# Optimization experiments

Hardware: AMD Instinct MI355X
Metric: run time of the kernel (lower is better)

The kernel has to match this reference:

```python
import jax, jax.numpy as jnp
import numpy as np

V = 1.0      # SinReLU scale (gin-configurable)
EPS = 1e-5   # LayerNorm eps

def sinrelu(x):
    return jnp.where(x >= 0, (x + jnp.sin(x)) * V, jnp.zeros_like(x))

def _cell(x, h, p):
    # ELTMcell: fused gated recurrent step. torch Linear weights are [out, in].
    gates = x @ p['xi'].T + h @ p['hi'].T + p['bhi']          # [B, 2H]
    i_g, h_g = jnp.split(gates, 2, axis=-1)
    ch = jax.nn.sigmoid(i_g) * jnp.tanh(h_g)                  # candidate hidden
    xn = jnp.tanh(x @ p['ox'].T)                              # only_x path
    hn = jnp.tanh(h @ p['oh'].T)                              # only_h path
    o = jax.nn.sigmoid(xn @ p['io'].T + hn @ p['ho'].T + ch @ p['cho'].T + p['bcho'])
    a = o @ p['a'].T
    b = o @ p['b'].T
    return a * xn + b * hn + (1.0 - a - b) * ch

def _forward(x, p0, p1, ln_g, ln_b):
    B = x.shape[1]
    H = p0['hi'].shape[1]
    def step(carry, xt):
        h0, h1 = carry
        h0 = _cell(xt, h0, p0)
        h1 = _cell(h0, h1, p1)
        return (h0, h1), h1
    init = (jnp.zeros((B, H), x.dtype), jnp.zeros((B, H), x.dtype))
    _, out = jax.lax.scan(step, init, x)      # [S, B, H]
    out = sinrelu(out)                        # dropout = identity (eval mode)
    mu = jnp.mean(out, axis=-1, keepdims=True)
    var = jnp.var(out, axis=-1, keepdims=True)
    return (out - mu) * jax.lax.rsqrt(var + EPS) * ln_g + ln_b

def setup_inputs() -> dict:
    S, B, D, H = 512, 128, 128, 512   # seq_len, batch, layer_size, hidden = multiple*layer_size
    keys = iter(jax.random.split(jax.random.key(0), 40))
    def w(o, i):
        return jax.random.normal(next(keys), (o, i), jnp.float32) * 0.05
    def bvec(o):
        return jax.random.normal(next(keys), (o,), jnp.float32) * 0.05
    inp = {'x': jax.random.normal(next(keys), (S, B, D), jnp.float32)}
    for l, din in ((0, D), (1, H)):
        inp[f'w{l}_xi'] = w(2 * H, din)
        inp[f'w{l}_hi'] = w(2 * H, H)
        inp[f'b{l}_hi'] = bvec(2 * H)
        inp[f'w{l}_ox'] = w(H, din)
        inp[f'w{l}_oh'] = w(H, H)
        inp[f'w{l}_io'] = w(H, H)
        inp[f'w{l}_ho'] = w(H, H)
        inp[f'w{l}_cho'] = w(H, H)
        inp[f'b{l}_cho'] = bvec(H)
        inp[f'w{l}_a'] = w(H, H)
        inp[f'w{l}_b'] = w(H, H)
    inp['ln_g'] = jnp.ones((H,), jnp.float32)
    inp['ln_b'] = jnp.zeros((H,), jnp.float32)
    return inp

def reference(x, w0_xi, w0_hi, b0_hi, w0_ox, w0_oh, w0_io, w0_ho, w0_cho, b0_cho, w0_a, w0_b,
              w1_xi, w1_hi, b1_hi, w1_ox, w1_oh, w1_io, w1_ho, w1_cho, b1_cho, w1_a, w1_b,
              ln_g, ln_b):
    p0 = dict(xi=w0_xi, hi=w0_hi, bhi=b0_hi, ox=w0_ox, oh=w0_oh, io=w0_io, ho=w0_ho,
              cho=w0_cho, bcho=b0_cho, a=w0_a, b=w0_b)
    p1 = dict(xi=w1_xi, hi=w1_hi, bhi=b1_hi, ox=w1_ox, oh=w1_oh, io=w1_io, ho=w1_ho,
              cho=w1_cho, bcho=b1_cho, a=w1_a, b=w1_b)
    return _forward(x, p0, p1, ln_g, ln_b)
```

## Files before the change

kernel.cpp:

```cpp
#include <hip/hip_runtime.h>
#include <hip/hip_bf16.h>

#define S_ 512
#define B_ 128
#define D_ 128
#define H_ 512
#define NB_ 256

#define PK_SA 159744
#define PK_B  5111808
#define PK_BS 98304
#define PK_C  8257536
#define PK_CS 65536
#define PK_TOT 10354688
#define APLANE 65536
#define ASZ    131072

#define SC1 4.8828125e-4f
#define SC2 2.384185791015625e-7f

typedef short bf16x8 __attribute__((ext_vector_type(8)));
typedef _Float16 f16x8 __attribute__((ext_vector_type(8)));
typedef int i32x4 __attribute__((ext_vector_type(4)));
typedef float f32x4 __attribute__((ext_vector_type(4)));

__device__ __forceinline__ float sigf(float x) { return 1.0f / (1.0f + expf(-x)); }

__device__ __forceinline__ i32x4 ldg(const short* p) {
  i32x4 o;
  asm volatile("global_load_dwordx4 %0, %1, off" : "=v"(o) : "v"(p));
  return o;
}
#define VMDRAIN()                                    \
  do {                                               \
    asm volatile("s_waitcnt vmcnt(0)" ::: "memory"); \
    __builtin_amdgcn_sched_barrier(0);               \
  } while (0)

__device__ __forceinline__ void st2(short* buf, int idx, float v) {
  _Float16 h0 = (_Float16)v;
  float r1 = (v - (float)h0) * 2048.0f;
  _Float16 h1 = (_Float16)r1;
  buf[idx] = __builtin_bit_cast(short, h0);
  buf[idx + APLANE] = __builtin_bit_cast(short, h1);
}
__device__ __forceinline__ float ld2p(const short* buf, int idx) {
  float a = (float)__builtin_bit_cast(_Float16, buf[idx]);
  float b = (float)__builtin_bit_cast(_Float16, buf[idx + APLANE]);
  return a + b * SC1;
}

#define MFMAH(a, b, c) __builtin_amdgcn_mfma_f32_16x16x32_f16(a, b, c, 0, 0, 0)
#define BC16(x) __builtin_bit_cast(f16x8, x)

__device__ __forceinline__ void mac4(f32x4& c0, f32x4& c1, f32x4& c2, const f16x8& a0,
                                     const f16x8& a1, const f16x8& w0, const f16x8& w1) {
  c0 = MFMAH(a0, w0, c0);
  c1 = MFMAH(a0, w1, c1);
  c1 = MFMAH(a1, w0, c1);
  c2 = MFMAH(a1, w1, c2);
}
__device__ __forceinline__ f32x4 fin3(const f32x4& c0, const f32x4& c1,
                                      const f32x4& c2) {
  f32x4 o;
#pragma unroll
  for (int e = 0; e < 4; ++e) o[e] = c0[e] + SC1 * c1[e] + SC2 * c2[e];
  return o;
}

__device__ __forceinline__ void unitP(f32x4& c0, f32x4& c1, f32x4& c2,
                                      const short* aBase, const short* slab, int nks,
                                      int lo) {
  for (int q = 0; q < nks; q += 4) {
    i32x4 A0[4], A1[4], W0[4], W1[4];
#pragma unroll
    for (int u = 0; u < 4; ++u) {
      const short* wp = slab + (size_t)(q + u) * 1024 + lo;
      W0[u] = ldg(wp);
      W1[u] = ldg(wp + 512);
      const short* ap = aBase + (q + u) * 32;
      A0[u] = ldg(ap);
      A1[u] = ldg(ap + APLANE);
    }
    VMDRAIN();
#pragma unroll
    for (int u = 0; u < 4; ++u)
      mac4(c0, c1, c2, BC16(A0[u]), BC16(A1[u]), BC16(W0[u]), BC16(W1[u]));
  }
}

__device__ __forceinline__ void unitPx(f32x4& c0, f32x4& c1, f32x4& c2,
                                       const float* xRow, const short* slab, int lo) {
  i32x4 W0[4], W1[4];
  f16x8 A0[4], A1[4];
#pragma unroll
  for (int u = 0; u < 4; ++u) {
    const short* wp = slab + (size_t)u * 1024 + lo;
    W0[u] = ldg(wp);
    W1[u] = ldg(wp + 512);
#pragma unroll
    for (int e = 0; e < 8; ++e) {
      float v = xRow[u * 32 + e];
      _Float16 h0 = (_Float16)v;
      A0[u][e] = h0;
      A1[u][e] = (_Float16)((v - (float)h0) * 2048.0f);
    }
  }
  VMDRAIN();
#pragma unroll
  for (int u = 0; u < 4; ++u) mac4(c0, c1, c2, A0[u], A1[u], BC16(W0[u]), BC16(W1[u]));
}

__device__ __forceinline__ unsigned int afa(unsigned int* p) {
  return __hip_atomic_fetch_add(p, 1u, __ATOMIC_RELAXED, __HIP_MEMORY_SCOPE_AGENT);
}
__device__ __forceinline__ unsigned int ald(const unsigned int* p) {
  return __hip_atomic_load(p, __ATOMIC_RELAXED, __HIP_MEMORY_SCOPE_AGENT);
}

__device__ __forceinline__ void gbarX(unsigned int* ctl, int xcd, unsigned int bt,
                                      unsigned int m) {
  asm volatile("s_waitcnt vmcnt(0) lgkmcnt(0)" ::: "memory");
  __syncthreads();
  if (threadIdx.x == 0) {
    unsigned int o = afa(&ctl[32 + 32 * xcd]);
    if (o == m * bt - 1)
      afa(&ctl[48 + 32 * xcd]);
    else
      while (ald(&ctl[48 + 32 * xcd]) < bt) __builtin_amdgcn_s_sleep(2);
  }
  __syncthreads();
  asm volatile("buffer_inv sc0" ::: "memory");
  __builtin_amdgcn_sched_barrier(0);
}

struct PP {
  const float* x;
  const short* pw;
  short* h0s;
  short* h1s;
  short* xn0;
  short* hn0;
  short* ch0;
  short* xn1;
  short* hn1;
  short* ch1;
  short* o0;
  short* o1;
  const float* bhi0;
  const float* bcho0;
  const float* bhi1;
  const float* bcho1;
  float* out;
  unsigned int* ctl;
};

__global__ __launch_bounds__(512, 1) void eltm_p(PP p) {
  extern __shared__ char smem[];
  float* ldsF = (float*)smem;
  unsigned int* shI = (unsigned int*)(smem + 16384);
  const int tid = threadIdx.x;
  const int lane = tid & 63;
  const int w = tid >> 6;
  const int r = lane & 15;
  const int g = lane >> 4;
  const int lo = r * 32 + g * 8;
  const f32x4 z = {0.f, 0.f, 0.f, 0.f};

  unsigned int xcd;
  asm volatile("s_getreg_b32 %0, hwreg(HW_REG_XCC_ID)" : "=s"(xcd));
  xcd &= 7;
  const int sgx = ((int)xcd) << 2;

  if (tid == 0) {
    shI[0] = afa(&p.ctl[xcd]);
    unsigned int o = afa(&p.ctl[8]);
    if (o == NB_ - 1)
      __hip_atomic_store(&p.ctl[9], 1u, __ATOMIC_RELAXED, __HIP_MEMORY_SCOPE_AGENT);
    while (ald(&p.ctl[9]) == 0) __builtin_amdgcn_s_sleep(2);
    shI[1] = ald(&p.ctl[xcd]);
  }
  __syncthreads();
  const int slot = shI[0];
  const unsigned int m = shI[1];
  asm volatile("buffer_inv sc0" ::: "memory");

  const int row0 = (int)xcd * 16;
  const int aoff = (row0 + r) * H_ + g * 8;
  static const int preW[8] = {0, 20480, 40960, 45056, 61440, 94208, 126976, 143360};

  unsigned int bt = 0;
  for (int i = 0; i <= S_; ++i) {
    const int do0 = i < S_;
    const int do1 = i >= 1;
    const float* xr = p.x + ((size_t)i * B_ + row0 + r) * D_ + g * 8;

    for (int t = slot; t < 32; t += (int)m) {
      const int s = (t + sgx) & 31;
      const short* slabA = p.pw + (size_t)s * PK_SA;
      const int n = s * 16 + r;
      f32x4 c0 = z, c1 = z, c2 = z;
      f32x4 fin = z;
      switch (w) {
        case 0:
        case 1:
          if (do0) {
            const short* sl = slabA + preW[w];
            unitPx(c0, c1, c2, xr, sl, lo);
            unitP(c0, c1, c2, p.h0s + aoff, sl + 4096, 16, lo);
            fin = fin3(c0, c1, c2);
          }
          break;
        case 2:
          if (do0) {
            unitPx(c0, c1, c2, xr, slabA + preW[2], lo);
            fin = fin3(c0, c1, c2);
#pragma unroll
            for (int e = 0; e < 4; ++e)
              st2(p.xn0, (row0 + g * 4 + e) * H_ + n, tanhf(fin[e]));
          }
          break;
        case 3:
          if (do0) {
            unitP(c0, c1, c2, p.h0s + aoff, slabA + preW[3], 16, lo);
            fin = fin3(c0, c1, c2);
#pragma unroll
            for (int e = 0; e < 4; ++e)
              st2(p.hn0, (row0 + g * 4 + e) * H_ + n, tanhf(fin[e]));
          }
          break;
        case 4:
        case 5:
          if (do1) {
            const short* sl = slabA + preW[w];
            unitP(c0, c1, c2, p.h0s + aoff, sl, 16, lo);
            unitP(c0, c1, c2, p.h1s + aoff, sl + 16384, 16, lo);
            fin = fin3(c0, c1, c2);
          }
          break;
        case 6:
          if (do1) {
            unitP(c0, c1, c2, p.h0s + aoff, slabA + preW[6], 16, lo);
            fin = fin3(c0, c1, c2);
#pragma unroll
            for (int e = 0; e < 4; ++e)
              st2(p.xn1, (row0 + g * 4 + e) * H_ + n, tanhf(fin[e]));
          }
          break;
        default:
          if (do1) {
            unitP(c0, c1, c2, p.h1s + aoff, slabA + preW[7], 16, lo);
            fin = fin3(c0, c1, c2);
#pragma unroll
            for (int e = 0; e < 4; ++e)
              st2(p.hn1, (row0 + g * 4 + e) * H_ + n, tanhf(fin[e]));
          }
          break;
      }
      if ((w == 1 && do0) || (w == 5 && do1)) {
#pragma unroll
        for (int e = 0; e < 4; ++e)
          ldsF[(w == 5 ? 256 : 0) + (g * 4 + e) * 16 + r] = fin[e];
      }
      __syncthreads();
      if (w == 0 && do0) {
        const float bi = p.bhi0[n], bh = p.bhi0[512 + n];
#pragma unroll
        for (int e = 0; e < 4; ++e) {
          float hgv = ldsF[(g * 4 + e) * 16 + r];
          st2(p.ch0, (row0 + g * 4 + e) * H_ + n, sigf(fin[e] + bi) * tanhf(hgv + bh));
        }
      }
      if (w == 4 && do1) {
        const float bi = p.bhi1[n], bh = p.bhi1[512 + n];
#pragma unroll
        for (int e = 0; e < 4; ++e) {
          float hgv = ldsF[256 + (g * 4 + e) * 16 + r];
          st2(p.ch1, (row0 + g * 4 + e) * H_ + n, sigf(fin[e] + bi) * tanhf(hgv + bh));
        }
      }
      __syncthreads();
    }
    ++bt;
    gbarX(p.ctl, xcd, bt, m);

    for (int t = slot; t < 32; t += (int)m) {
      const int s = (t + sgx) & 31;
      const int L = w >> 2;
      const int tt = w & 3;
      const int ok = L ? do1 : do0;
      const int n = s * 16 + r;
      if (ok) {
        f32x4 c0 = z, c1 = z, c2 = z;
        const short* slab = p.pw + PK_B + (size_t)s * PK_BS + (size_t)L * 49152;
        const short* xn = L ? p.xn1 : p.xn0;
        const short* hn = L ? p.hn1 : p.hn0;
        const short* ch = L ? p.ch1 : p.ch0;
        if (tt == 0)
          unitP(c0, c1, c2, xn + aoff, slab, 16, lo);
        else if (tt == 1)
          unitP(c0, c1, c2, hn + aoff, slab + 16384, 16, lo);
        else if (tt == 2)
          unitP(c0, c1, c2, ch + aoff, slab + 32768, 8, lo);
        else
          unitP(c0, c1, c2, ch + aoff + 256, slab + 40960, 8, lo);
        f32x4 fin = fin3(c0, c1, c2);
#pragma unroll
        for (int e = 0; e < 4; ++e) ldsF[w * 256 + (g * 4 + e) * 16 + r] = fin[e];
      }
      __syncthreads();
      if ((w == 0 && do0) || (w == 4 && do1)) {
        const float bc = (w == 4 ? p.bcho1 : p.bcho0)[n];
        short* o = w == 4 ? p.o1 : p.o0;
#pragma unroll
        for (int e = 0; e < 4; ++e) {
          const int q = (g * 4 + e) * 16 + r;
          float sum = ldsF[w * 256 + q] + ldsF[(w + 1) * 256 + q] +
                      ldsF[(w + 2) * 256 + q] + ldsF[(w + 3) * 256 + q];
          st2(o, (row0 + g * 4 + e) * H_ + n, sigf(sum + bc));
        }
      }
      __syncthreads();
    }
    ++bt;
    gbarX(p.ctl, xcd, bt, m);

    for (int t = slot; t < 32; t += (int)m) {
      const int s = (t + sgx) & 31;
      const int L = s & 1;
      const int ok = L ? do1 : do0;
      const int u = w >> 1;
      const int h = w & 1;
      if (ok) {
        f32x4 c0 = z, c1 = z, c2 = z;
        const short* slab =
            p.pw + PK_C + (size_t)s * PK_CS + (size_t)u * 16384 + (size_t)h * 8192;
        const short* o = L ? p.o1 : p.o0;
        unitP(c0, c1, c2, o + aoff + h * 256, slab, 8, lo);
        f32x4 fin = fin3(c0, c1, c2);
#pragma unroll
        for (int e = 0; e < 4; ++e) ldsF[w * 256 + (g * 4 + e) * 16 + r] = fin[e];
      }
      __syncthreads();
      if ((w == 0 || w == 4) && ok) {
        const int j = (w == 0) ? (s >> 1) : (16 + (s >> 1));
        const int ub = (w == 0) ? 0 : 4;
        const short* xn = L ? p.xn1 : p.xn0;
        const short* hn = L ? p.hn1 : p.hn0;
        const short* ch = L ? p.ch1 : p.ch0;
        short* hs = L ? p.h1s : p.h0s;
#pragma unroll
        for (int e = 0; e < 4; ++e) {
          const int q = (g * 4 + e) * 16 + r;
          const float av = ldsF[(ub + 0) * 256 + q] + ldsF[(ub + 1) * 256 + q];
          const float bv = ldsF[(ub + 2) * 256 + q] + ldsF[(ub + 3) * 256 + q];
          const int idx = (row0 + g * 4 + e) * H_ + j * 16 + r;
          const float hval = av * ld2p(xn, idx) + bv * ld2p(hn, idx) +
                             (1.f - av - bv) * ld2p(ch, idx);
          st2(hs, idx, hval);
          if (L) p.out[(size_t)(i - 1) * B_ * H_ + idx] = hval;
        }
      }
      __syncthreads();
    }
    ++bt;
    gbarX(p.ctl, xcd, bt, m);
  }
}

struct WP18 {
  const float* m[18];
};
__global__ void repack(WP18 wp, short* pw) {
  const long long t8 = (long long)blockIdx.x * 256 + threadIdx.x;
  const long long id = t8 * 8;
  if (id >= (long long)PK_TOT) return;
  int mat, row, kb, p;
  if (id < (long long)PK_B) {
    int s = (int)(id / PK_SA), rem = (int)(id % PK_SA);
    const int pre[9] = {0, 20480, 40960, 45056, 61440, 94208, 126976, 143360, 159744};
    int w = 0;
    while (rem >= pre[w + 1]) ++w;
    int off = rem - pre[w];
    int c = off >> 10, r2 = off & 1023;
    p = r2 >> 9;
    int q2 = r2 & 511, rr = q2 >> 5, gg = (q2 & 31) >> 3;
    int kin = c * 32 + gg * 8;
    switch (w) {
      case 0:
      case 1:
        row = (w == 1 ? 512 : 0) + s * 16 + rr;
        if (kin < 128) { mat = 0; kb = kin; } else { mat = 1; kb = kin - 128; }
        break;
      case 2: mat = 2; row = s * 16 + rr; kb = kin; break;
      case 3: mat = 3; row = s * 16 + rr; kb = kin; break;
      case 4:
      case 5:
        row = (w == 5 ? 512 : 0) + s * 16 + rr;
        if (kin < 512) { mat = 9; kb = kin; } else { mat = 10; kb = kin - 512; }
        break;
      case 6: mat = 11; row = s * 16 + rr; kb = kin; break;
      default: mat = 12; row = s * 16 + rr; kb = kin; break;
    }
  } else if (id < (long long)PK_C) {
    int rem = (int)(id - PK_B);
    int s = rem / PK_BS, r2 = rem % PK_BS;
    int tt = r2 / 16384, off = r2 % 16384;
    int c = off >> 10, r3 = off & 1023;
    p = r3 >> 9;
    int q2 = r3 & 511, rr = q2 >> 5, gg = (q2 & 31) >> 3;
    const int mats[6] = {4, 5, 6, 13, 14, 15};
    mat = mats[tt];
    row = s * 16 + rr;
    kb = c * 32 + gg * 8;
  } else {
    int rem = (int)(id - PK_C);
    int s = rem / PK_CS, r2 = rem % PK_CS;
    int u = r2 / 16384, off = r2 % 16384;
    int c = off >> 10, r3 = off & 1023;
    p = r3 >> 9;
    int q2 = r3 & 511, rr = q2 >> 5, gg = (q2 & 31) >> 3;
    int L = s & 1, j = (u < 2) ? (s >> 1) : (16 + (s >> 1));
    mat = (L ? 16 : 7) + (u & 1);
    row = j * 16 + rr;
    kb = c * 32 + gg * 8;
  }
  const int KS = (mat == 0 || mat == 2) ? 128 : 512;
  const float* src = wp.m[mat] + (long long)row * KS + kb;
  bf16x8 o8;
#pragma unroll
  for (int e = 0; e < 8; ++e) {
    float v = src[e];
    _Float16 h0 = (_Float16)v;
    short sv;
    if (p == 0) {
      sv = __builtin_bit_cast(short, h0);
    } else {
      _Float16 h1 = (_Float16)((v - (float)h0) * 2048.0f);
      sv = __builtin_bit_cast(short, h1);
    }
    o8[e] = sv;
  }
  *(bf16x8*)(pw + id) = o8;
}

__global__ void eltm_kLN(float* __restrict__ out, const float* __restrict__ g,
                         const float* __restrict__ bta) {
  const int row = blockIdx.x * 4 + (threadIdx.x >> 6);
  const int lane = threadIdx.x & 63;
  float* r = out + (size_t)row * H_;
  float v[8];
  float s = 0.f, s2 = 0.f;
#pragma unroll
  for (int i = 0; i < 8; ++i) {
    float x = r[lane + i * 64];
    float sv = (x >= 0.f) ? (x + sinf(x)) : 0.f;
    v[i] = sv;
    s += sv;
    s2 += sv * sv;
  }
#pragma unroll
  for (int m = 1; m < 64; m <<= 1) {
    s += __shfl_xor(s, m);
    s2 += __shfl_xor(s2, m);
  }
  const float mean = s * (1.f / 512.f);
  const float var = s2 * (1.f / 512.f) - mean * mean;
  const float rstd = rsqrtf(var + 1e-5f);
#pragma unroll
  for (int i = 0; i < 8; ++i) {
    const int c = lane + i * 64;
    r[c] = (v[i] - mean) * rstd * g[c] + bta[c];
  }
}

extern "C" void kernel_launch(void* const* d_in, const int* in_sizes, int n_in,
                              void* d_out, int out_size, void* d_ws, size_t ws_size,
                              hipStream_t stream) {
#define W(i) ((const float*)d_in[i])
  short* pw = (short*)d_ws;
  short* acts = pw + (size_t)PK_TOT;
  short* h0s = acts;
  short* h1s = acts + ASZ;
  short* xn0 = acts + 2 * ASZ;
  short* hn0 = acts + 3 * ASZ;
  short* ch0 = acts + 4 * ASZ;
  short* xn1 = acts + 5 * ASZ;
  short* hn1 = acts + 6 * ASZ;
  short* ch1 = acts + 7 * ASZ;
  short* o0 = acts + 8 * ASZ;
  short* o1 = acts + 9 * ASZ;
  unsigned int* ctl = (unsigned int*)(acts + 10 * (size_t)ASZ);
  float* out = (float*)d_out;

  WP18 wps;
  const int srcIdx[18] = {1, 2, 4, 5, 6, 7, 8, 10, 11, 12, 13, 15, 16, 17, 18, 19, 21, 22};
  for (int i = 0; i < 18; ++i) wps.m[i] = W(srcIdx[i]);

  repack<<<PK_TOT / 8 / 256, 256, 0, stream>>>(wps, pw);
  hipMemsetAsync(h0s, 0, (size_t)2 * ASZ * sizeof(short), stream);
  hipMemsetAsync(ctl, 0, 2048, stream);

  hipFuncSetAttribute((const void*)eltm_p, hipFuncAttributeMaxDynamicSharedMemorySize,
                      98304);
  PP pa;
  pa.x = (const float*)d_in[0];
  pa.pw = pw;
  pa.h0s = h0s;
  pa.h1s = h1s;
  pa.xn0 = xn0;
  pa.hn0 = hn0;
  pa.ch0 = ch0;
  pa.xn1 = xn1;
  pa.hn1 = hn1;
  pa.ch1 = ch1;
  pa.o0 = o0;
  pa.o1 = o1;
  pa.bhi0 = W(3);
  pa.bcho0 = W(9);
  pa.bhi1 = W(14);
  pa.bcho1 = W(20);
  pa.out = out;
  pa.ctl = ctl;
  eltm_p<<<NB_, 512, 98304, stream>>>(pa);

  eltm_kLN<<<16384, 256, 0, stream>>>(out, W(23), W(24));
#undef W
}
```

Measured before the change: 20.95 ms.

## Replace per-XCD dynamic slot scheduling with static block mapping and hierarchical barrier

The change drops the dynamic slot assignment based on XCC_ID and fixes each block to one slab and one row group derived from blockIdx. The weight repack now keeps all three phase slabs contiguous per slab index. The per-XCD barrier becomes a two-level global barrier: 8 groups of 32, then a master counter, with a timeout guard. Activation stores now use sc1 global stores and the barrier invalidates with buffer_inv sc1, so activations exchanged between phases are coherent device-wide. The aim is to remove the scheduling loop overhead and improve weight locality, at the cost of a wider barrier that spans every XCD.

```diff
diff --git a/kernel.cpp b/kernel.cpp
--- a/kernel.cpp
+++ b/kernel.cpp
@@ -7,17 +7,13 @@
 #define H_ 512
 #define NB_ 256
 
-#define PK_SA 159744
-#define PK_B  5111808
-#define PK_BS 98304
-#define PK_C  8257536
-#define PK_CS 65536
+#define SLAB_SHORTS 323584
 #define PK_TOT 10354688
 #define APLANE 65536
 #define ASZ    131072
 
-#define SC1 4.8828125e-4f
-#define SC2 2.384185791015625e-7f
+#define SC1F 4.8828125e-4f
+#define SC2F 2.384185791015625e-7f
 
 typedef short bf16x8 __attribute__((ext_vector_type(8)));
 typedef _Float16 f16x8 __attribute__((ext_vector_type(8)));
@@ -37,17 +33,19 @@
     __builtin_amdgcn_sched_barrier(0);               \
   } while (0)
 
-__device__ __forceinline__ void st2(short* buf, int idx, float v) {
+__device__ __forceinline__ void stg16s(short* p, unsigned int v) {
+  asm volatile("global_store_short %0, %1, off sc1" ::"v"(p), "v"(v) : "memory");
+}
+__device__ __forceinline__ void st2sc(short* buf, int idx, float v) {
   _Float16 h0 = (_Float16)v;
-  float r1 = (v - (float)h0) * 2048.0f;
-  _Float16 h1 = (_Float16)r1;
-  buf[idx] = __builtin_bit_cast(short, h0);
-  buf[idx + APLANE] = __builtin_bit_cast(short, h1);
+  _Float16 h1 = (_Float16)((v - (float)h0) * 2048.0f);
+  stg16s(buf + idx, (unsigned int)__builtin_bit_cast(unsigned short, h0));
+  stg16s(buf + idx + APLANE, (unsigned int)__builtin_bit_cast(unsigned short, h1));
 }
 __device__ __forceinline__ float ld2p(const short* buf, int idx) {
   float a = (float)__builtin_bit_cast(_Float16, buf[idx]);
   float b = (float)__builtin_bit_cast(_Float16, buf[idx + APLANE]);
-  return a + b * SC1;
+  return a + b * SC1F;
 }
 
 #define MFMAH(a, b, c) __builtin_amdgcn_mfma_f32_16x16x32_f16(a, b, c, 0, 0, 0)
@@ -64,7 +62,7 @@
                                       const f32x4& c2) {
   f32x4 o;
 #pragma unroll
-  for (int e = 0; e < 4; ++e) o[e] = c0[e] + SC1 * c1[e] + SC2 * c2[e];
+  for (int e = 0; e < 4; ++e) o[e] = c0[e] + SC1F * c1[e] + SC2F * c2[e];
   return o;
 }
 
@@ -118,19 +116,24 @@
   return __hip_atomic_load(p, __ATOMIC_RELAXED, __HIP_MEMORY_SCOPE_AGENT);
 }
 
-__device__ __forceinline__ void gbarX(unsigned int* ctl, int xcd, unsigned int bt,
-                                      unsigned int m) {
+__device__ __forceinline__ void gbar(unsigned int* ctl, unsigned int t, int grp) {
   asm volatile("s_waitcnt vmcnt(0) lgkmcnt(0)" ::: "memory");
   __syncthreads();
   if (threadIdx.x == 0) {
-    unsigned int o = afa(&ctl[32 + 32 * xcd]);
-    if (o == m * bt - 1)
-      afa(&ctl[48 + 32 * xcd]);
-    else
-      while (ald(&ctl[48 + 32 * xcd]) < bt) __builtin_amdgcn_s_sleep(2);
+    unsigned int a = afa(&ctl[grp * 32]);
+    if (a == t * 32u - 1u) {
+      unsigned int m = afa(&ctl[256]);
+      if (m == t * 8u - 1u)
+        __hip_atomic_store(&ctl[288], t, __ATOMIC_RELAXED, __HIP_MEMORY_SCOPE_AGENT);
+    }
+    int guard = 0;
+    while (ald(&ctl[288]) < t) {
+      __builtin_amdgcn_s_sleep(2);
+      if (++guard > (1 << 24)) break;
+    }
   }
   __syncthreads();
-  asm volatile("buffer_inv sc0" ::: "memory");
+  asm volatile("buffer_inv sc1" ::: "memory");
   __builtin_amdgcn_sched_barrier(0);
 }
 
@@ -158,7 +161,6 @@
 __global__ __launch_bounds__(512, 1) void eltm_p(PP p) {
   extern __shared__ char smem[];
   float* ldsF = (float*)smem;
-  unsigned int* shI = (unsigned int*)(smem + 16384);
   const int tid = threadIdx.x;
   const int lane = tid & 63;
   const int w = tid >> 6;
@@ -167,26 +169,13 @@
   const int lo = r * 32 + g * 8;
   const f32x4 z = {0.f, 0.f, 0.f, 0.f};
 
-  unsigned int xcd;
-  asm volatile("s_getreg_b32 %0, hwreg(HW_REG_XCC_ID)" : "=s"(xcd));
-  xcd &= 7;
-  const int sgx = ((int)xcd) << 2;
-
-  if (tid == 0) {
-    shI[0] = afa(&p.ctl[xcd]);
-    unsigned int o = afa(&p.ctl[8]);
-    if (o == NB_ - 1)
-      __hip_atomic_store(&p.ctl[9], 1u, __ATOMIC_RELAXED, __HIP_MEMORY_SCOPE_AGENT);
-    while (ald(&p.ctl[9]) == 0) __builtin_amdgcn_s_sleep(2);
-    shI[1] = ald(&p.ctl[xcd]);
-  }
-  __syncthreads();
-  const int slot = shI[0];
-  const unsigned int m = shI[1];
-  asm volatile("buffer_inv sc0" ::: "memory");
-
-  const int row0 = (int)xcd * 16;
+  const int bid = blockIdx.x;
+  const int s = (bid & 7) * 4 + (bid >> 6);
+  const int row0 = ((bid >> 3) & 7) * 16;
+  const int grp = bid & 7;
+
   const int aoff = (row0 + r) * H_ + g * 8;
+  const int n = s * 16 + r;
   static const int preW[8] = {0, 20480, 40960, 45056, 61440, 94208, 126976, 143360};
 
   unsigned int bt = 0;
@@ -194,11 +183,9 @@
     const int do0 = i < S_;
     const int do1 = i >= 1;
     const float* xr = p.x + ((size_t)i * B_ + row0 + r) * D_ + g * 8;
-
-    for (int t = slot; t < 32; t += (int)m) {
-      const int s = (t + sgx) & 31;
-      const short* slabA = p.pw + (size_t)s * PK_SA;
-      const int n = s * 16 + r;
+    const short* slabA = p.pw + (size_t)s * SLAB_SHORTS;
+
+    {
       f32x4 c0 = z, c1 = z, c2 = z;
       f32x4 fin = z;
       switch (w) {
@@ -217,7 +204,7 @@
             fin = fin3(c0, c1, c2);
 #pragma unroll
             for (int e = 0; e < 4; ++e)
-              st2(p.xn0, (row0 + g * 4 + e) * H_ + n, tanhf(fin[e]));
+              st2sc(p.xn0, (row0 + g * 4 + e) * H_ + n, tanhf(fin[e]));
           }
           break;
         case 3:
@@ -226,7 +213,7 @@
             fin = fin3(c0, c1, c2);
 #pragma unroll
             for (int e = 0; e < 4; ++e)
-              st2(p.hn0, (row0 + g * 4 + e) * H_ + n, tanhf(fin[e]));
+              st2sc(p.hn0, (row0 + g * 4 + e) * H_ + n, tanhf(fin[e]));
           }
           break;
         case 4:
@@ -244,7 +231,7 @@
             fin = fin3(c0, c1, c2);
 #pragma unroll
             for (int e = 0; e < 4; ++e)
-              st2(p.xn1, (row0 + g * 4 + e) * H_ + n, tanhf(fin[e]));
+              st2sc(p.xn1, (row0 + g * 4 + e) * H_ + n, tanhf(fin[e]));
           }
           break;
         default:
@@ -253,7 +240,7 @@
             fin = fin3(c0, c1, c2);
 #pragma unroll
             for (int e = 0; e < 4; ++e)
-              st2(p.hn1, (row0 + g * 4 + e) * H_ + n, tanhf(fin[e]));
+              st2sc(p.hn1, (row0 + g * 4 + e) * H_ + n, tanhf(fin[e]));
           }
           break;
       }
@@ -268,7 +255,7 @@
 #pragma unroll
         for (int e = 0; e < 4; ++e) {
           float hgv = ldsF[(g * 4 + e) * 16 + r];
-          st2(p.ch0, (row0 + g * 4 + e) * H_ + n, sigf(fin[e] + bi) * tanhf(hgv + bh));
+          st2sc(p.ch0, (row0 + g * 4 + e) * H_ + n, sigf(fin[e] + bi) * tanhf(hgv + bh));
         }
       }
       if (w == 4 && do1) {
@@ -276,23 +263,23 @@
 #pragma unroll
         for (int e = 0; e < 4; ++e) {
           float hgv = ldsF[256 + (g * 4 + e) * 16 + r];
-          st2(p.ch1, (row0 + g * 4 + e) * H_ + n, sigf(fin[e] + bi) * tanhf(hgv + bh));
+          st2sc(p.ch1, (row0 + g * 4 + e) * H_ + n, sigf(fin[e] + bi) * tanhf(hgv + bh));
         }
       }
       __syncthreads();
     }
     ++bt;
-    gbarX(p.ctl, xcd, bt, m);
-
-    for (int t = slot; t < 32; t += (int)m) {
-      const int s = (t + sgx) & 31;
+    gbar(p.ctl, bt, grp);
+
+    {
       const int L = w >> 2;
       const int tt = w & 3;
       const int ok = L ? do1 : do0;
-      const int n = s * 16 + r;
+      f32x4 fA = z;
       if (ok) {
         f32x4 c0 = z, c1 = z, c2 = z;
-        const short* slab = p.pw + PK_B + (size_t)s * PK_BS + (size_t)L * 49152;
+        const short* slab =
+            p.pw + (size_t)s * SLAB_SHORTS + 156 * 1024 + (size_t)L * 49152;
         const short* xn = L ? p.xn1 : p.xn0;
         const short* hn = L ? p.hn1 : p.hn0;
         const short* ch = L ? p.ch1 : p.ch0;
@@ -304,9 +291,9 @@
           unitP(c0, c1, c2, ch + aoff, slab + 32768, 8, lo);
         else
           unitP(c0, c1, c2, ch + aoff + 256, slab + 40960, 8, lo);
-        f32x4 fin = fin3(c0, c1, c2);
-#pragma unroll
-        for (int e = 0; e < 4; ++e) ldsF[w * 256 + (g * 4 + e) * 16 + r] = fin[e];
+        fA = fin3(c0, c1, c2);
+#pragma unroll
+        for (int e = 0; e < 4; ++e) ldsF[w * 256 + (g * 4 + e) * 16 + r] = fA[e];
       }
       __syncthreads();
       if ((w == 0 && do0) || (w == 4 && do1)) {
@@ -317,24 +304,23 @@
           const int q = (g * 4 + e) * 16 + r;
           float sum = ldsF[w * 256 + q] + ldsF[(w + 1) * 256 + q] +
                       ldsF[(w + 2) * 256 + q] + ldsF[(w + 3) * 256 + q];
-          st2(o, (row0 + g * 4 + e) * H_ + n, sigf(sum + bc));
+          st2sc(o, (row0 + g * 4 + e) * H_ + n, sigf(sum + bc));
         }
       }
       __syncthreads();
     }
     ++bt;
-    gbarX(p.ctl, xcd, bt, m);
-
-    for (int t = slot; t < 32; t += (int)m) {
-      const int s = (t + sgx) & 31;
+    gbar(p.ctl, bt, grp);
+
+    {
       const int L = s & 1;
       const int ok = L ? do1 : do0;
       const int u = w >> 1;
       const int h = w & 1;
       if (ok) {
         f32x4 c0 = z, c1 = z, c2 = z;
-        const short* slab =
-            p.pw + PK_C + (size_t)s * PK_CS + (size_t)u * 16384 + (size_t)h * 8192;
+        const short* slab = p.pw + (size_t)s * SLAB_SHORTS + 252 * 1024 +
+                            (size_t)u * 16384 + (size_t)h * 8192;
         const short* o = L ? p.o1 : p.o0;
         unitP(c0, c1, c2, o + aoff + h * 256, slab, 8, lo);
         f32x4 fin = fin3(c0, c1, c2);
@@ -357,14 +343,14 @@
           const int idx = (row0 + g * 4 + e) * H_ + j * 16 + r;
           const float hval = av * ld2p(xn, idx) + bv * ld2p(hn, idx) +
                              (1.f - av - bv) * ld2p(ch, idx);
-          st2(hs, idx, hval);
+          st2sc(hs, idx, hval);
           if (L) p.out[(size_t)(i - 1) * B_ * H_ + idx] = hval;
         }
       }
       __syncthreads();
     }
     ++bt;
-    gbarX(p.ctl, xcd, bt, m);
+    gbar(p.ctl, bt, grp);
   }
 }
 
@@ -375,55 +361,59 @@
   const long long t8 = (long long)blockIdx.x * 256 + threadIdx.x;
   const long long id = t8 * 8;
   if (id >= (long long)PK_TOT) return;
-  int mat, row, kb, p;
-  if (id < (long long)PK_B) {
-    int s = (int)(id / PK_SA), rem = (int)(id % PK_SA);
-    const int pre[9] = {0, 20480, 40960, 45056, 61440, 94208, 126976, 143360, 159744};
-    int w = 0;
-    while (rem >= pre[w + 1]) ++w;
-    int off = rem - pre[w];
-    int c = off >> 10, r2 = off & 1023;
-    p = r2 >> 9;
-    int q2 = r2 & 511, rr = q2 >> 5, gg = (q2 & 31) >> 3;
-    int kin = c * 32 + gg * 8;
-    switch (w) {
+  const int s = (int)(id / SLAB_SHORTS);
+  const int rem = (int)(id % SLAB_SHORTS);
+  const int c = rem >> 10;
+  const int r2 = rem & 1023;
+  const int p = r2 >> 9;
+  const int q2 = r2 & 511;
+  const int rr = q2 >> 5;
+  const int gg = (q2 & 31) >> 3;
+  const int n0 = s * 16;
+  int mat, row, kb;
+  if (c < 156) {
+    const int segA[9] = {0, 20, 40, 44, 60, 92, 124, 140, 156};
+    int sg = 0;
+    while (c >= segA[sg + 1]) ++sg;
+    const int cl = c - segA[sg];
+    const int kin = cl * 32 + gg * 8;
+    switch (sg) {
       case 0:
-      case 1:
-        row = (w == 1 ? 512 : 0) + s * 16 + rr;
+        row = n0 + rr;
         if (kin < 128) { mat = 0; kb = kin; } else { mat = 1; kb = kin - 128; }
         break;
-      case 2: mat = 2; row = s * 16 + rr; kb = kin; break;
-      case 3: mat = 3; row = s * 16 + rr; kb = kin; break;
+      case 1:
+        row = 512 + n0 + rr;
+        if (kin < 128) { mat = 0; kb = kin; } else { mat = 1; kb = kin - 128; }
+        break;
+      case 2: mat = 2; row = n0 + rr; kb = kin; break;
+      case 3: mat = 3; row = n0 + rr; kb = kin; break;
       case 4:
-      case 5:
-        row = (w == 5 ? 512 : 0) + s * 16 + rr;
+        row = n0 + rr;
         if (kin < 512) { mat = 9; kb = kin; } else { mat = 10; kb = kin - 512; }
         break;
-      case 6: mat = 11; row = s * 16 + rr; kb = kin; break;
-      default: mat = 12; row = s * 16 + rr; kb = kin; break;
-    }
-  } else if (id < (long long)PK_C) {
-    int rem = (int)(id - PK_B);
-    int s = rem / PK_BS, r2 = rem % PK_BS;
-    int tt = r2 / 16384, off = r2 % 16384;
-    int c = off >> 10, r3 = off & 1023;
-    p = r3 >> 9;
-    int q2 = r3 & 511, rr = q2 >> 5, gg = (q2 & 31) >> 3;
-    const int mats[6] = {4, 5, 6, 13, 14, 15};
-    mat = mats[tt];
-    row = s * 16 + rr;
-    kb = c * 32 + gg * 8;
+      case 5:
+        row = 512 + n0 + rr;
+        if (kin < 512) { mat = 9; kb = kin; } else { mat = 10; kb = kin - 512; }
+        break;
+      case 6: mat = 11; row = n0 + rr; kb = kin; break;
+      default: mat = 12; row = n0 + rr; kb = kin; break;
+    }
+  } else if (c < 252) {
+    const int cl = c - 156;
+    const int L = cl >= 48;
+    const int cc = cl - (L ? 48 : 0);
+    mat = (L ? 13 : 4) + (cc >> 4);
+    row = n0 + rr;
+    kb = (cc & 15) * 32 + gg * 8;
   } else {
-    int rem = (int)(id - PK_C);
-    int s = rem / PK_CS, r2 = rem % PK_CS;
-    int u = r2 / 16384, off = r2 % 16384;
-    int c = off >> 10, r3 = off & 1023;
-    p = r3 >> 9;
-    int q2 = r3 & 511, rr = q2 >> 5, gg = (q2 & 31) >> 3;
-    int L = s & 1, j = (u < 2) ? (s >> 1) : (16 + (s >> 1));
+    const int cc = c - 252;
+    const int u = cc >> 4;
+    const int L = s & 1;
+    const int j = (u < 2) ? (s >> 1) : (16 + (s >> 1));
     mat = (L ? 16 : 7) + (u & 1);
     row = j * 16 + rr;
-    kb = c * 32 + gg * 8;
+    kb = (cc & 15) * 32 + gg * 8;
   }
   const int KS = (mat == 0 || mat == 2) ? 128 : 512;
   const float* src = wp.m[mat] + (long long)row * KS + kb;
@@ -433,9 +423,9 @@
     float v = src[e];
     _Float16 h0 = (_Float16)v;
     short sv;
-    if (p == 0) {
+    if (p == 0)
       sv = __builtin_bit_cast(short, h0);
-    } else {
+    else {
       _Float16 h1 = (_Float16)((v - (float)h0) * 2048.0f);
       sv = __builtin_bit_cast(short, h1);
     }
@@ -494,12 +484,13 @@
   float* out = (float*)d_out;
 
   WP18 wps;
-  const int srcIdx[18] = {1, 2, 4, 5, 6, 7, 8, 10, 11, 12, 13, 15, 16, 17, 18, 19, 21, 22};
+  const int srcIdx[18] = {1,  2,  4,  5,  6,  7,  8,  10, 11,
+                          12, 13, 15, 16, 17, 18, 19, 21, 22};
   for (int i = 0; i < 18; ++i) wps.m[i] = W(srcIdx[i]);
 
   repack<<<PK_TOT / 8 / 256, 256, 0, stream>>>(wps, pw);
   hipMemsetAsync(h0s, 0, (size_t)2 * ASZ * sizeof(short), stream);
-  hipMemsetAsync(ctl, 0, 2048, stream);
+  hipMemsetAsync(ctl, 0, 4096, stream);
 
   hipFuncSetAttribute((const void*)eltm_p, hipFuncAttributeMaxDynamicSharedMemorySize,
                       98304);
```

Measured after the change: 51.62 ms. +146.5%, slower.
